# Performance work log

Hardware: AMD Instinct MI355X
Metric: run time of the kernel (lower is better)

## Reference

```python
import jax, jax.numpy as jnp
import numpy as np

T, B, DIN, H, C = 32, 256, 4196, 1024, 151
DROP_P = 0.2


def setup_inputs() -> dict:
    key = jax.random.key(0)
    ks = jax.random.split(key, 9)
    x = jax.random.normal(ks[0], (T, B, DIN), dtype=jnp.float32)
    h0 = jnp.zeros((B, H), dtype=jnp.float32)
    c0 = jnp.zeros((B, H), dtype=jnp.float32)
    # recurrent dropout mask: binary mask scaled by 1/(1-p), sampled once, reused per step
    keep = (jax.random.uniform(ks[1], (B, H)) > DROP_P).astype(jnp.float32)
    dropout_mask = keep / (1.0 - DROP_P)
    s_in = 1.0 / np.sqrt(DIN)
    s_st = 1.0 / np.sqrt(H)
    W_in = jax.random.normal(ks[2], (6 * H, DIN), dtype=jnp.float32) * s_in
    b_in = jnp.zeros((6 * H,), dtype=jnp.float32)
    W_state = jax.random.normal(ks[3], (5 * H, H), dtype=jnp.float32) * s_st
    # bias init: zeros except forget-gate chunk = 1.0 (reset_parameters)
    b_state = jnp.zeros((5 * H,), dtype=jnp.float32).at[H:2 * H].set(1.0)
    W_out = jax.random.normal(ks[4], (C, H), dtype=jnp.float32) * s_st
    b_out = jnp.zeros((C,), dtype=jnp.float32)
    return {"x": x, "h0": h0, "c0": c0, "dropout_mask": dropout_mask,
            "W_in": W_in, "b_in": b_in, "W_state": W_state, "b_state": b_state,
            "W_out": W_out, "b_out": b_out}


def reference(x, h0, c0, dropout_mask, W_in, b_in, W_state, b_state, W_out, b_out):
    def step(carry, xt):
        h, c = carry
        pi = xt @ W_in.T + b_in            # [B, 6H]
        ps = h @ W_state.T + b_state       # [B, 5H]
        i_g = jax.nn.sigmoid(pi[:, 0 * H:1 * H] + ps[:, 0 * H:1 * H])
        f_g = jax.nn.sigmoid(pi[:, 1 * H:2 * H] + ps[:, 1 * H:2 * H])
        m_i = jnp.tanh(pi[:, 2 * H:3 * H] + ps[:, 2 * H:3 * H])
        o_g = jax.nn.sigmoid(pi[:, 3 * H:4 * H] + ps[:, 3 * H:4 * H])
        mem = i_g * m_i + f_g * c
        out = o_g * jnp.tanh(mem)
        hw = jax.nn.sigmoid(pi[:, 4 * H:5 * H] + ps[:, 4 * H:5 * H])
        out = hw * out + (1.0 - hw) * pi[:, 5 * H:6 * H]
        out = out * dropout_mask
        return (out, mem), out

    (_, _), hs = jax.lax.scan(step, (h0, c0), x)   # hs: [T, B, H]
    logits = jnp.einsum('tbh,ch->tbc', hs, W_out) + b_out
    return logits
```

## Files before the change

kernel.cpp:

```cpp
#include <hip/hip_runtime.h>
#include <hip/hip_bf16.h>
#include <cstdio>

typedef __bf16 bf16;
typedef __bf16 bf16x8 __attribute__((ext_vector_type(8)));
typedef __bf16 bf16x4 __attribute__((ext_vector_type(4)));
typedef float f32x4 __attribute__((ext_vector_type(4)));

__device__ __forceinline__ float sigmoidf_(float x) { return 1.f / (1.f + __expf(-x)); }
__device__ __forceinline__ float tanhf_(float x)    { return 1.f - 2.f / (__expf(2.f * x) + 1.f); }

__device__ __forceinline__ void gld_lds16(const bf16* g, bf16* l) {
    __builtin_amdgcn_global_load_lds(
        (const __attribute__((address_space(1))) void*)g,
        (__attribute__((address_space(3))) void*)l, 16, 0, 0);
}

template<int BM, int BN, bool OUTBF16, bool NBOUND>
__global__ __launch_bounds__(256)
void gemm_lds_k(const bf16* __restrict__ A, const bf16* __restrict__ B,
                void* __restrict__ Cv, const float* __restrict__ bias,
                int K, int lda, int ldb, int ldc, int Nlim)
{
    constexpr int TM = BM / 32;
    constexpr int TN = BN / 32;

    __shared__ __align__(16) bf16 As[BM * 64];
    __shared__ __align__(16) bf16 Bs[BN * 64];

    const int tid  = threadIdx.x;
    const int wave = tid >> 6;
    const int lane = tid & 63;
    const int lrow = lane & 15;
    const int q    = lane >> 4;

    const int rowbase = blockIdx.y * BM;
    const int colbase = blockIdx.x * BN;
    const int wr = (wave >> 1) * (BM / 2);
    const int wc = (wave & 1) * (BN / 2);

    f32x4 acc[TM][TN] = {};

    for (int kk = 0; kk < K; kk += 64) {
        __syncthreads();
        #pragma unroll
        for (int i = 0; i < BM / 32; ++i) {
            int c  = tid + i * 256;
            int r  = c >> 3;
            int sl = c & 7;
            int ks = (sl ^ (r & 7)) * 8;
            gld_lds16(A + (size_t)(rowbase + r) * lda + kk + ks, &As[c * 8]);
        }
        #pragma unroll
        for (int i = 0; i < BN / 32; ++i) {
            int c  = tid + i * 256;
            int r  = c >> 3;
            int sl = c & 7;
            int ks = (sl ^ (r & 7)) * 8;
            gld_lds16(B + (size_t)(colbase + r) * ldb + kk + ks, &Bs[c * 8]);
        }
        __syncthreads();

        #pragma unroll
        for (int ks = 0; ks < 2; ++ks) {
            bf16x8 afr[TM], bfr[TN];
            #pragma unroll
            for (int m = 0; m < TM; ++m) {
                int r = wr + m * 16 + lrow;
                int s = ((ks << 2) | q) ^ (r & 7);
                afr[m] = *(const bf16x8*)&As[r * 64 + s * 8];
            }
            #pragma unroll
            for (int n = 0; n < TN; ++n) {
                int r = wc + n * 16 + lrow;
                int s = ((ks << 2) | q) ^ (r & 7);
                bfr[n] = *(const bf16x8*)&Bs[r * 64 + s * 8];
            }
            #pragma unroll
            for (int m = 0; m < TM; ++m)
                #pragma unroll
                for (int n = 0; n < TN; ++n)
                    acc[m][n] = __builtin_amdgcn_mfma_f32_16x16x32_bf16(
                                    afr[m], bfr[n], acc[m][n], 0, 0, 0);
        }
    }

    #pragma unroll
    for (int m = 0; m < TM; ++m) {
        #pragma unroll
        for (int n = 0; n < TN; ++n) {
            int gr0 = rowbase + wr + m * 16 + q * 4;
            int gc  = colbase + wc + n * 16 + lrow;
            bool cok = (!NBOUND) || (gc < Nlim);
            float bv = cok ? bias[gc] : 0.f;
            #pragma unroll
            for (int rix = 0; rix < 4; ++rix) {
                if (cok) {
                    float v = acc[m][n][rix] + bv;
                    size_t o = (size_t)(gr0 + rix) * ldc + gc;
                    if (OUTBF16) ((bf16*)Cv)[o] = (bf16)v;
                    else         ((float*)Cv)[o] = v;
                }
            }
        }
    }
}

template<int BM, int BN>
__global__ __launch_bounds__(256)
void gemm_cast_k(const float* __restrict__ Av, const float* __restrict__ Bv,
                 bf16* __restrict__ Cv, const float* __restrict__ bias,
                 int K, int Klim, int lda, int ldb, int ldc)
{
    constexpr int TM = BM / 32;
    constexpr int TN = BN / 32;
    constexpr int LDK = 40;

    __shared__ __align__(16) bf16 As[BM * LDK];
    __shared__ __align__(16) bf16 Bs[BN * LDK];

    const int tid  = threadIdx.x;
    const int wave = tid >> 6;
    const int lane = tid & 63;
    const int lrow = lane & 15;
    const int q    = lane >> 4;

    const int rowbase = blockIdx.y * BM;
    const int colbase = blockIdx.x * BN;
    const int wr = (wave >> 1) * (BM / 2);
    const int wc = (wave & 1) * (BN / 2);

    f32x4 acc[TM][TN] = {};

    for (int kk = 0; kk < K; kk += 32) {
        __syncthreads();
        #pragma unroll
        for (int i = 0; i < BM / 64; ++i) {
            int c = tid + i * 256;
            int r = c >> 2, kc = (c & 3) * 8, kg = kk + kc;
            const float* src = Av + (size_t)(rowbase + r) * lda + kg;
            bf16x8 v;
            if (kg + 8 <= Klim) {
                float4 f0 = *(const float4*)(src);
                float4 f1 = *(const float4*)(src + 4);
                v[0]=(bf16)f0.x; v[1]=(bf16)f0.y; v[2]=(bf16)f0.z; v[3]=(bf16)f0.w;
                v[4]=(bf16)f1.x; v[5]=(bf16)f1.y; v[6]=(bf16)f1.z; v[7]=(bf16)f1.w;
            } else {
                #pragma unroll
                for (int e = 0; e < 8; ++e) v[e] = (kg + e < Klim) ? (bf16)src[e] : (bf16)0.f;
            }
            *(bf16x8*)&As[r * LDK + kc] = v;
        }
        #pragma unroll
        for (int i = 0; i < BN / 64; ++i) {
            int c = tid + i * 256;
            int r = c >> 2, kc = (c & 3) * 8, kg = kk + kc;
            const float* src = Bv + (size_t)(colbase + r) * ldb + kg;
            bf16x8 v;
            if (kg + 8 <= Klim) {
                float4 f0 = *(const float4*)(src);
                float4 f1 = *(const float4*)(src + 4);
                v[0]=(bf16)f0.x; v[1]=(bf16)f0.y; v[2]=(bf16)f0.z; v[3]=(bf16)f0.w;
                v[4]=(bf16)f1.x; v[5]=(bf16)f1.y; v[6]=(bf16)f1.z; v[7]=(bf16)f1.w;
            } else {
                #pragma unroll
                for (int e = 0; e < 8; ++e) v[e] = (kg + e < Klim) ? (bf16)src[e] : (bf16)0.f;
            }
            *(bf16x8*)&Bs[r * LDK + kc] = v;
        }
        __syncthreads();

        bf16x8 afr[TM], bfr[TN];
        #pragma unroll
        for (int m = 0; m < TM; ++m)
            afr[m] = *(const bf16x8*)&As[(wr + m * 16 + lrow) * LDK + q * 8];
        #pragma unroll
        for (int n = 0; n < TN; ++n)
            bfr[n] = *(const bf16x8*)&Bs[(wc + n * 16 + lrow) * LDK + q * 8];
        #pragma unroll
        for (int m = 0; m < TM; ++m)
            #pragma unroll
            for (int n = 0; n < TN; ++n)
                acc[m][n] = __builtin_amdgcn_mfma_f32_16x16x32_bf16(
                                afr[m], bfr[n], acc[m][n], 0, 0, 0);
    }

    #pragma unroll
    for (int m = 0; m < TM; ++m) {
        #pragma unroll
        for (int n = 0; n < TN; ++n) {
            int gr0 = rowbase + wr + m * 16 + q * 4;
            int gc  = colbase + wc + n * 16 + lrow;
            float bv = bias[gc];
            #pragma unroll
            for (int rix = 0; rix < 4; ++rix)
                Cv[(size_t)(gr0 + rix) * ldc + gc] = (bf16)(acc[m][n][rix] + bv);
        }
    }
}

__global__ __launch_bounds__(512)
void step_k2(const bf16*  __restrict__ hprev,
             const bf16*  __restrict__ wsb,
             const bf16*  __restrict__ pi_t,
             const float* __restrict__ b_state,
             float*       __restrict__ cst,
             const float* __restrict__ dmask,
             bf16*        __restrict__ hnext)
{
    __shared__ __align__(16) unsigned char smem[36864];
    bf16* Asb = (bf16*)smem;
    bf16* Bsb = (bf16*)(smem + 16384);
    float* red = (float*)smem;

    const int tid   = threadIdx.x;
    const int wv    = tid >> 6;
    const int g2    = wv >> 2;
    const int wg    = wv & 3;
    const int lane  = tid & 63;
    const int lrow  = lane & 15;
    const int q     = lane >> 4;
    const int lt    = tid & 255;

    const int lb    = blockIdx.x;
    const int hb    = (lb >> 5) * 8 + (lb & 7);
    const int hbase = hb * 16;
    const int bbase = ((lb >> 3) & 3) * 64;
    const int kbase = g2 * 512;

    bf16* Ag = Asb + g2 * 4096;
    bf16* Bg = Bsb + g2 * 5120;

    const int b0   = bbase + wg * 16 + q * 4;
    const int hcol = hbase + lrow;
    bf16  pif[4][6];
    float crv[4], dmv[4], bsv[5];
    if (g2 == 0) {
        #pragma unroll
        for (int rix = 0; rix < 4; ++rix) {
            const bf16* pib = pi_t + (size_t)(b0 + rix) * 6144 + hcol;
            #pragma unroll
            for (int g = 0; g < 6; ++g) pif[rix][g] = pib[g * 1024];
            size_t j = (size_t)(b0 + rix) * 1024 + hcol;
            crv[rix] = cst[j];
            dmv[rix] = dmask[j];
        }
        #pragma unroll
        for (int g = 0; g < 5; ++g) bsv[g] = b_state[g * 1024 + hcol];
    }

    f32x4 acc[5] = {};
    for (int it = 0; it < 8; ++it) {
        const int kb = kbase + it * 64;
        __syncthreads();
        #pragma unroll
        for (int i = 0; i < 2; ++i) {
            int c  = lt + i * 256;
            int r  = c >> 3, sl = c & 7;
            int ks = (sl ^ (r & 7)) * 8;
            gld_lds16(hprev + (size_t)(bbase + r) * 1024 + kb + ks, Ag + c * 8);
        }
        #pragma unroll
        for (int i = 0; i < 3; ++i) {
            int c = lt + i * 256;
            if (c < 640) {
                int r  = c >> 3, sl = c & 7;
                int g  = r >> 4, hh = r & 15;
                int ks = (sl ^ (r & 7)) * 8;
                gld_lds16(wsb + (size_t)(g * 1024 + hbase + hh) * 1024 + kb + ks,
                          Bg + c * 8);
            }
        }
        __syncthreads();

        #pragma unroll
        for (int ks = 0; ks < 2; ++ks) {
            int ra = wg * 16 + lrow;
            int sa = ((ks << 2) | q) ^ (ra & 7);
            bf16x8 af = *(const bf16x8*)&Ag[ra * 64 + sa * 8];
            #pragma unroll
            for (int g = 0; g < 5; ++g) {
                int rb = g * 16 + lrow;
                int sb = ((ks << 2) | q) ^ (rb & 7);
                bf16x8 bv = *(const bf16x8*)&Bg[rb * 64 + sb * 8];
                acc[g] = __builtin_amdgcn_mfma_f32_16x16x32_bf16(af, bv, acc[g], 0, 0, 0);
            }
        }
    }

    __syncthreads();
    if (g2 == 1) {
        #pragma unroll
        for (int g = 0; g < 5; ++g)
            *(f32x4*)&red[(lt * 5 + g) * 4] = acc[g];
    }
    __syncthreads();
    if (g2 == 0) {
        #pragma unroll
        for (int g = 0; g < 5; ++g)
            acc[g] += *(const f32x4*)&red[(lt * 5 + g) * 4];

        #pragma unroll
        for (int rix = 0; rix < 4; ++rix) {
            int b = b0 + rix;
            float p0 = acc[0][rix] + bsv[0] + (float)pif[rix][0];
            float p1 = acc[1][rix] + bsv[1] + (float)pif[rix][1];
            float p2 = acc[2][rix] + bsv[2] + (float)pif[rix][2];
            float p3 = acc[3][rix] + bsv[3] + (float)pif[rix][3];
            float p4 = acc[4][rix] + bsv[4] + (float)pif[rix][4];
            float p5 = (float)pif[rix][5];

            float ig = sigmoidf_(p0);
            float fg = sigmoidf_(p1);
            float mi = tanhf_(p2);
            float og = sigmoidf_(p3);
            float hw = sigmoidf_(p4);

            size_t j = (size_t)b * 1024 + hcol;
            float mem = ig * mi + fg * crv[rix];
            cst[j] = mem;
            float out = og * tanhf_(mem);
            out = hw * out + (1.f - hw) * p5;
            out *= dmv[rix];
            hnext[j] = (bf16)out;
        }
    }
}

__global__ void cast_f2b4_k(const float* __restrict__ src, bf16* __restrict__ dst, int n4) {
    int i = blockIdx.x * 256 + threadIdx.x;
    if (i < n4) {
        float4 f = *(const float4*)(src + i * 4);
        bf16x4 v; v[0]=(bf16)f.x; v[1]=(bf16)f.y; v[2]=(bf16)f.z; v[3]=(bf16)f.w;
        *(bf16x4*)(dst + i * 4) = v;
    }
}

__global__ void cast_wout_k(const float* __restrict__ src, bf16* __restrict__ dst, int Crows) {
    int i = blockIdx.x * 256 + threadIdx.x;
    int r = i >> 10;
    dst[i] = (r < Crows) ? (bf16)src[i] : (bf16)0.f;
}

__global__ void cast_pad4_k(const float* __restrict__ src, bf16* __restrict__ dst,
                            int klim, int kp) {
    int r = blockIdx.x;
    const float* s = src + (size_t)r * klim;
    bf16* d = dst + (size_t)r * kp;
    int nk4 = kp >> 2, lim4 = klim >> 2;
    for (int c = threadIdx.x; c < nk4; c += 256) {
        bf16x4 v;
        if (c < lim4) {
            float4 f = *(const float4*)(s + c * 4);
            v[0]=(bf16)f.x; v[1]=(bf16)f.y; v[2]=(bf16)f.z; v[3]=(bf16)f.w;
        } else {
            v[0]=v[1]=v[2]=v[3]=(bf16)0.f;
        }
        *(bf16x4*)(d + c * 4) = v;
    }
}

__global__ void init_state_k(const float* __restrict__ c0, const float* __restrict__ h0,
                             float* __restrict__ cst, bf16* __restrict__ hs0) {
    int i = blockIdx.x * 256 + threadIdx.x;
    cst[i] = c0[i];
    hs0[i] = (bf16)h0[i];
}

extern "C" void kernel_launch(void* const* d_in, const int* in_sizes, int n_in,
                              void* d_out, int out_size, void* d_ws, size_t ws_size,
                              hipStream_t stream)
{
    const float* x       = (const float*)d_in[0];
    const float* h0      = (const float*)d_in[1];
    const float* c0      = (const float*)d_in[2];
    const float* dmask   = (const float*)d_in[3];
    const float* W_in    = (const float*)d_in[4];
    const float* b_in    = (const float*)d_in[5];
    const float* W_state = (const float*)d_in[6];
    const float* b_state = (const float*)d_in[7];
    const float* W_out   = (const float*)d_in[8];
    const float* b_out   = (const float*)d_in[9];

    constexpr int T = 32, B = 256, DIN = 4196, H = 1024, C = 151;
    constexpr int M  = T * B;
    constexpr int KP = 4224;
    constexpr int N6 = 6 * H;
    constexpr int N5 = 5 * H;

    size_t off = 0;
    auto carve = [&](size_t bytes) -> void* {
        void* p = (char*)d_ws + off;
        off += (bytes + 255) & ~(size_t)255;
        return p;
    };
    bf16*  pi  = (bf16*) carve((size_t)M * N6 * 2);
    bf16*  wsb = (bf16*) carve((size_t)N5 * H * 2);
    bf16*  wob = (bf16*) carve((size_t)192 * H * 2);
    bf16*  hs  = (bf16*) carve((size_t)(T + 1) * B * H * 2);
    float* cst = (float*)carve((size_t)B * H * 4);
    size_t base_need = off;

    bf16 *xb = nullptr, *wb = nullptr;
    bool precast = (ws_size >= base_need + (size_t)M * KP * 2 + (size_t)N6 * KP * 2 + 1024);
    if (precast) {
        xb = (bf16*)carve((size_t)M * KP * 2);
        wb = (bf16*)carve((size_t)N6 * KP * 2);
    }
    if (ws_size < base_need) {
        fprintf(stderr, "kernel_launch: ws too small (%zu < %zu)\n", ws_size, base_need);
        return;
    }

    hipLaunchKernelGGL(cast_f2b4_k, dim3((N5 * H / 4 + 255) / 256), dim3(256), 0, stream,
                       W_state, wsb, N5 * H / 4);
    hipLaunchKernelGGL(cast_wout_k, dim3(192 * H / 256), dim3(256), 0, stream, W_out, wob, C);
    hipLaunchKernelGGL(init_state_k, dim3(B * H / 256), dim3(256), 0, stream, c0, h0, cst, hs);

    if (precast) {
        hipLaunchKernelGGL(cast_pad4_k, dim3(M),  dim3(256), 0, stream, x,    xb, DIN, KP);
        hipLaunchKernelGGL(cast_pad4_k, dim3(N6), dim3(256), 0, stream, W_in, wb, DIN, KP);
        hipLaunchKernelGGL((gemm_lds_k<128, 128, true, false>),
                           dim3(N6 / 128, M / 128), dim3(256), 0, stream,
                           xb, wb, pi, b_in, KP, KP, KP, N6, N6);
    } else {
        hipLaunchKernelGGL((gemm_cast_k<128, 128>),
                           dim3(N6 / 128, M / 128), dim3(256), 0, stream,
                           x, W_in, pi, b_in, KP, DIN, DIN, DIN, N6);
    }

    for (int t = 0; t < T; ++t) {
        hipLaunchKernelGGL(step_k2, dim3(256), dim3(512), 0, stream,
                           hs + (size_t)t * B * H, wsb,
                           pi + (size_t)t * B * N6, b_state,
                           cst, dmask,
                           hs + (size_t)(t + 1) * B * H);
    }

    hipLaunchKernelGGL((gemm_lds_k<128, 64, false, true>),
                       dim3(192 / 64, M / 128), dim3(256), 0, stream,
                       hs + (size_t)B * H, wob, (float*)d_out, b_out,
                       H, H, H, C, C);
}
```

Measured before the change: 1.144 ms.

## Replace input-projection GEMM with 256x256 double-buffered 8-wave MFMA kernel

Replaces the 128x128 LDS GEMM for the input projection with a 256x256-tile kernel using 512 threads. It double-buffers LDS, interleaves async global-to-LDS staging with MFMA phases, applies an XOR-swizzled LDS layout, and remaps blocks so neighbouring blocks share tiles. The aim is higher arithmetic intensity and better overlap of loads with compute for the large x@W_in^T GEMM. It uses 128KB of LDS per block and many accumulator registers, which limits occupancy. The grid has only 32x24 blocks, so tail effects are possible.

New measurement: 1.103 ms. 3.6% less time.

```diff
diff --git a/kernel.cpp b/kernel.cpp
--- a/kernel.cpp
+++ b/kernel.cpp
@@ -14,6 +14,135 @@
     __builtin_amdgcn_global_load_lds(
         (const __attribute__((address_space(1))) void*)g,
         (__attribute__((address_space(3))) void*)l, 16, 0, 0);
+}
+
+__device__ __forceinline__ bf16x8 ldsfrag(const bf16* buf, int r, int kq) {
+    int s = kq ^ (r & 7);
+    return *(const bf16x8*)&buf[r * 64 + s * 8];
+}
+
+__device__ __forceinline__ void stage64(const bf16* src, int ld, int kk,
+                                        bf16* dst, int r0, int tid) {
+    int r  = r0 + (tid >> 3);
+    int sl = tid & 7;
+    int ks = (sl ^ (r & 7)) * 8;
+    gld_lds16(src + (size_t)r * ld + kk + ks, dst + (r0 * 8 + tid) * 8);
+}
+
+__global__ __launch_bounds__(512)
+void gemm256_k(const bf16* __restrict__ A, const bf16* __restrict__ B,
+               bf16* __restrict__ C, const float* __restrict__ bias,
+               int K, int lda, int ldb, int ldc, int nbx)
+{
+    __shared__ __align__(16) bf16 As[2][256 * 64];
+    __shared__ __align__(16) bf16 Bs[2][256 * 64];
+
+    const int tid  = threadIdx.x;
+    const int wave = tid >> 6;
+    const int lane = tid & 63;
+    const int lrow = lane & 15;
+    const int q    = lane >> 4;
+
+    const int lb  = blockIdx.x;
+    const int cpx = gridDim.x >> 3;
+    const int swz = (lb & 7) * cpx + (lb >> 3);
+    const int bx  = swz % nbx;
+    const int by  = swz / nbx;
+
+    const int rowbase = by * 256;
+    const int colbase = bx * 256;
+    const int wr = (wave >> 2) * 128;
+    const int wc = (wave & 3) * 64;
+
+    const bf16* Ab = A + (size_t)rowbase * lda;
+    const bf16* Bb = B + (size_t)colbase * ldb;
+
+    f32x4 acc[8][4] = {};
+    const int NT = K >> 6;
+
+#define G256_STAGE(ph, buf_, kk_)                                              \
+    do {                                                                       \
+        if ((ph) == 0) { stage64(Bb, ldb, (kk_), Bs[buf_],   0, tid);          \
+                         stage64(Bb, ldb, (kk_), Bs[buf_],  64, tid); }        \
+        if ((ph) == 1) { stage64(Bb, ldb, (kk_), Bs[buf_], 128, tid);          \
+                         stage64(Bb, ldb, (kk_), Bs[buf_], 192, tid); }        \
+        if ((ph) == 2) { stage64(Ab, lda, (kk_), As[buf_],   0, tid);          \
+                         stage64(Ab, lda, (kk_), As[buf_], 128, tid); }        \
+        if ((ph) == 3) { stage64(Ab, lda, (kk_), As[buf_],  64, tid);          \
+                         stage64(Ab, lda, (kk_), As[buf_], 192, tid); }        \
+    } while (0)
+
+#define G256_PHASE(ph)                                                         \
+    do {                                                                       \
+        bf16x8 a00 = ldsfrag(Ac, wr + (2 * (ph) + 0) * 16 + lrow, q);          \
+        bf16x8 a01 = ldsfrag(Ac, wr + (2 * (ph) + 0) * 16 + lrow, 4 | q);      \
+        bf16x8 a10 = ldsfrag(Ac, wr + (2 * (ph) + 1) * 16 + lrow, q);          \
+        bf16x8 a11 = ldsfrag(Ac, wr + (2 * (ph) + 1) * 16 + lrow, 4 | q);      \
+        G256_STAGE(ph, nb, kkn);                                               \
+        __builtin_amdgcn_s_barrier();                                          \
+        __builtin_amdgcn_s_setprio(1);                                         \
+        _Pragma("unroll")                                                      \
+        for (int n_ = 0; n_ < 4; ++n_) {                                       \
+            acc[2 * (ph) + 0][n_] = __builtin_amdgcn_mfma_f32_16x16x32_bf16(   \
+                a00, bfr[n_][0], acc[2 * (ph) + 0][n_], 0, 0, 0);              \
+            acc[2 * (ph) + 0][n_] = __builtin_amdgcn_mfma_f32_16x16x32_bf16(   \
+                a01, bfr[n_][1], acc[2 * (ph) + 0][n_], 0, 0, 0);              \
+            acc[2 * (ph) + 1][n_] = __builtin_amdgcn_mfma_f32_16x16x32_bf16(   \
+                a10, bfr[n_][0], acc[2 * (ph) + 1][n_], 0, 0, 0);              \
+            acc[2 * (ph) + 1][n_] = __builtin_amdgcn_mfma_f32_16x16x32_bf16(   \
+                a11, bfr[n_][1], acc[2 * (ph) + 1][n_], 0, 0, 0);              \
+        }                                                                      \
+        __builtin_amdgcn_s_setprio(0);                                         \
+    } while (0)
+
+    G256_STAGE(0, 0, 0);
+    G256_STAGE(1, 0, 0);
+    G256_STAGE(2, 0, 0);
+    G256_STAGE(3, 0, 0);
+    asm volatile("s_waitcnt vmcnt(2)\n\ts_barrier" ::: "memory");
+
+    for (int t = 0; t < NT; ++t) {
+        const int cb  = t & 1;
+        const int nb  = cb ^ 1;
+        const int tn  = (t + 1 < NT) ? (t + 1) : t;
+        const int kkn = tn << 6;
+        const bf16* Ac = As[cb];
+        const bf16* Bc = Bs[cb];
+
+        bf16x8 bfr[4][2];
+        #pragma unroll
+        for (int n = 0; n < 4; ++n) {
+            int rb = wc + n * 16 + lrow;
+            bfr[n][0] = ldsfrag(Bc, rb, q);
+            bfr[n][1] = ldsfrag(Bc, rb, 4 | q);
+        }
+
+        G256_PHASE(0);
+        __builtin_amdgcn_s_barrier();
+        G256_PHASE(1);
+        asm volatile("s_waitcnt vmcnt(4)\n\ts_barrier" ::: "memory");
+        G256_PHASE(2);
+        __builtin_amdgcn_s_barrier();
+        G256_PHASE(3);
+        asm volatile("s_waitcnt vmcnt(2)\n\ts_barrier" ::: "memory");
+    }
+    asm volatile("s_waitcnt vmcnt(0)" ::: "memory");
+
+#undef G256_PHASE
+#undef G256_STAGE
+
+    #pragma unroll
+    for (int m = 0; m < 8; ++m) {
+        #pragma unroll
+        for (int n = 0; n < 4; ++n) {
+            int gr0 = rowbase + wr + m * 16 + q * 4;
+            int gc  = colbase + wc + n * 16 + lrow;
+            float bv = bias[gc];
+            #pragma unroll
+            for (int rix = 0; rix < 4; ++rix)
+                C[(size_t)(gr0 + rix) * ldc + gc] = (bf16)(acc[m][n][rix] + bv);
+        }
+    }
 }
 
 template<int BM, int BN, bool OUTBF16, bool NBOUND>
@@ -420,9 +549,9 @@
     if (precast) {
         hipLaunchKernelGGL(cast_pad4_k, dim3(M),  dim3(256), 0, stream, x,    xb, DIN, KP);
         hipLaunchKernelGGL(cast_pad4_k, dim3(N6), dim3(256), 0, stream, W_in, wb, DIN, KP);
-        hipLaunchKernelGGL((gemm_lds_k<128, 128, true, false>),
-                           dim3(N6 / 128, M / 128), dim3(256), 0, stream,
-                           xb, wb, pi, b_in, KP, KP, KP, N6, N6);
+        hipLaunchKernelGGL(gemm256_k,
+                           dim3((M / 256) * (N6 / 256)), dim3(512), 0, stream,
+                           xb, wb, pi, b_in, KP, KP, KP, N6, N6 / 256);
     } else {
         hipLaunchKernelGGL((gemm_cast_k<128, 128>),
                            dim3(N6 / 128, M / 128), dim3(256), 0, stream,
```
